# Performance work log

Measured on AMD Instinct MI355X. Metric: run time of the kernel, lower is better.

Reference implementation:

```python
import jax, jax.numpy as jnp
import numpy as np

VOCAB = 100000
D = 128
B = 256
L = 2048  # leaves per tree (power of two -> complete binary tree)


def setup_inputs() -> dict:
    key = jax.random.key(0)
    k1, k2, k3, k4 = jax.random.split(key, 4)
    word_ids = jax.random.randint(k1, (B, L), 0, VOCAB)
    embedding = jax.random.normal(k2, (VOCAB, D), dtype=jnp.float32) * 0.1
    # torch nn.Linear(2*D, D): weight [D, 2*D], bias [D]
    W = jax.random.normal(k3, (D, 2 * D), dtype=jnp.float32) * (1.0 / np.sqrt(2 * D))
    b = jax.random.normal(k4, (D,), dtype=jnp.float32) * 0.01
    return {"word_ids": word_ids, "embedding": embedding, "W": W, "b": b}


def reference(word_ids, embedding, W, b):
    # Leaves: embedding lookup for every leaf of every tree. [B, L, D]
    x = embedding[word_ids]
    # Internal nodes, batched by depth: each level combines adjacent pairs
    # via linear(concat(left, right)). log2(L) levels (static unroll).
    while x.shape[1] > 1:
        left = x[:, 0::2, :]   # [B, n/2, D]
        right = x[:, 1::2, :]  # [B, n/2, D]
        pair = jnp.concatenate([left, right], axis=-1)  # [B, n/2, 2D]
        x = jnp.einsum('bnd,od->bno', pair, W) + b      # [B, n/2, D]
    return x[:, 0, :]  # root result per tree, [B, D]
```

## Files before the change

### kernel.cpp

```cpp
#include <hip/hip_runtime.h>


typedef __bf16 bf16x8 __attribute__((ext_vector_type(8)));
typedef __bf16 bf16x4 __attribute__((ext_vector_type(4)));
typedef float f32x4 __attribute__((ext_vector_type(4)));

#define STRIDE 136

__global__ void pack_w_kernel(const float* __restrict__ W,
                              __bf16* __restrict__ wpack) {
    const int f = blockIdx.x;
    const int tid = threadIdx.x;
    const int wv = tid >> 6, l = tid & 63;
    const int nl = f >> 3, kk = f & 7;
    const int o = ((wv << 1) + nl) * 16 + (l & 15);
    const int d = kk * 32 + ((l >> 4) << 3);
    const float* src = W + o * 256 + d;
    bf16x8 h;
#pragma unroll
    for (int j = 0; j < 8; ++j) h[j] = (__bf16)src[j];
    *(bf16x8*)(wpack + (size_t)(f * 256 + tid) * 8) = h;
}

__device__ __forceinline__ void step32(
    const __bf16* src0, const __bf16* src1, __bf16* dst,
    const bf16x8* wf, const float* bval, int wv, int q, int lm)
{
    f32x4 acc[2][2];
#pragma unroll
    for (int mt = 0; mt < 2; ++mt)
#pragma unroll
        for (int nl = 0; nl < 2; ++nl)
            acc[mt][nl] = f32x4{ bval[nl], bval[nl], bval[nl], bval[nl] };
#pragma unroll
    for (int kh = 0; kh < 2; ++kh) {
        const int row = 2 * lm + kh;
        bf16x8 a0[4], a1[4];
#pragma unroll
        for (int j = 0; j < 4; ++j) {
            a0[j] = *(const bf16x8*)&src0[row * STRIDE + j * 32 + q * 8];
            a1[j] = *(const bf16x8*)&src1[row * STRIDE + j * 32 + q * 8];
        }
#pragma unroll
        for (int j = 0; j < 4; ++j) {
            acc[0][0] = __builtin_amdgcn_mfma_f32_16x16x32_bf16(
                a0[j], wf[0 * 8 + kh * 4 + j], acc[0][0], 0, 0, 0);
            acc[1][0] = __builtin_amdgcn_mfma_f32_16x16x32_bf16(
                a1[j], wf[0 * 8 + kh * 4 + j], acc[1][0], 0, 0, 0);
            acc[0][1] = __builtin_amdgcn_mfma_f32_16x16x32_bf16(
                a0[j], wf[1 * 8 + kh * 4 + j], acc[0][1], 0, 0, 0);
            acc[1][1] = __builtin_amdgcn_mfma_f32_16x16x32_bf16(
                a1[j], wf[1 * 8 + kh * 4 + j], acc[1][1], 0, 0, 0);
        }
    }
#pragma unroll
    for (int mt = 0; mt < 2; ++mt)
#pragma unroll
        for (int nl = 0; nl < 2; ++nl) {
            const int col = (2 * wv + nl) * 16 + lm;
            const bf16x4 hv = __builtin_convertvector(acc[mt][nl], bf16x4);
#pragma unroll
            for (int r = 0; r < 4; ++r)
                dst[(mt * 16 + q * 4 + r) * STRIDE + col] = hv[r];
        }
    __syncthreads();
}

template <int NOUT>
__device__ __forceinline__ void step_small(
    const __bf16* src, __bf16* dst,
    const bf16x8* wf, const float* bval, int wv, int q, int lm)
{
    const int me = (NOUT >= 16) ? lm : (lm < NOUT ? lm : 0);
    f32x4 acc[2];
    acc[0] = f32x4{ bval[0], bval[0], bval[0], bval[0] };
    acc[1] = f32x4{ bval[1], bval[1], bval[1], bval[1] };
#pragma unroll
    for (int kh = 0; kh < 2; ++kh) {
        const int row = 2 * me + kh;
        bf16x8 af[4];
#pragma unroll
        for (int j = 0; j < 4; ++j)
            af[j] = *(const bf16x8*)&src[row * STRIDE + j * 32 + q * 8];
#pragma unroll
        for (int nl = 0; nl < 2; ++nl)
#pragma unroll
            for (int j = 0; j < 4; ++j)
                acc[nl] = __builtin_amdgcn_mfma_f32_16x16x32_bf16(
                    af[j], wf[nl * 8 + kh * 4 + j], acc[nl], 0, 0, 0);
    }
#pragma unroll
    for (int nl = 0; nl < 2; ++nl) {
        const int col = (2 * wv + nl) * 16 + lm;
        const bf16x4 hv = __builtin_convertvector(acc[nl], bf16x4);
#pragma unroll
        for (int r = 0; r < 4; ++r) {
            const int row = q * 4 + r;
            if (row < NOUT)
                dst[row * STRIDE + col] = hv[r];
        }
    }
    __syncthreads();
}

__device__ __forceinline__ void final4(
    const __bf16* src, __bf16* yrow,
    const bf16x8* wf, const float* bval, int wv, int q, int lm)
{
    const int me = (lm < 4) ? lm : 0;
    f32x4 acc[2];
    acc[0] = f32x4{ bval[0], bval[0], bval[0], bval[0] };
    acc[1] = f32x4{ bval[1], bval[1], bval[1], bval[1] };
#pragma unroll
    for (int kh = 0; kh < 2; ++kh) {
        const int row = 2 * me + kh;
        bf16x8 af[4];
#pragma unroll
        for (int j = 0; j < 4; ++j)
            af[j] = *(const bf16x8*)&src[row * STRIDE + j * 32 + q * 8];
#pragma unroll
        for (int nl = 0; nl < 2; ++nl)
#pragma unroll
            for (int j = 0; j < 4; ++j)
                acc[nl] = __builtin_amdgcn_mfma_f32_16x16x32_bf16(
                    af[j], wf[nl * 8 + kh * 4 + j], acc[nl], 0, 0, 0);
    }
#pragma unroll
    for (int nl = 0; nl < 2; ++nl) {
        const int col = (2 * wv + nl) * 16 + lm;
        if (q == 0) {
#pragma unroll
            for (int r = 0; r < 4; ++r)
                yrow[r * 128 + col] = (__bf16)acc[nl][r];
        }
    }
}

__device__ __forceinline__ void gather_issue(
    const int* wb64, const float* emb, int tid, f32x4 (&s)[8])
{
#pragma unroll
    for (int i = 0; i < 8; ++i) {
        const int id = wb64[(tid >> 5) + 8 * i];
        s[i] = *(const f32x4*)(emb + (size_t)id * 128 + (tid & 31) * 4);
    }
}

__device__ __forceinline__ void gather_write(
    __bf16* dst, int tid, const f32x4 (&s)[8])
{
#pragma unroll
    for (int i = 0; i < 8; ++i) {
        const int row = (tid >> 5) + 8 * i;
        *(bf16x4*)&dst[row * STRIDE + (tid & 31) * 4] =
            __builtin_convertvector(s[i], bf16x4);
    }
}

__global__ __launch_bounds__(256, 3) void tree128_kernel(
    const int* __restrict__ wid, const float* __restrict__ emb,
    const __bf16* __restrict__ wpack, const float* __restrict__ bias,
    __bf16* __restrict__ yout)
{
    __shared__ __align__(16) __bf16 bufA[64 * STRIDE];
    __shared__ __align__(16) __bf16 bufB[64 * STRIDE];
    __shared__ __align__(16) __bf16 bufD[64 * STRIDE];
    const int tid = threadIdx.x;
    const int batch = blockIdx.x >> 3;
    const int pair = blockIdx.x & 7;
    const int wv = tid >> 6, ln = tid & 63, q = ln >> 4, lm = ln & 15;

    bf16x8 wf[16];
    const bf16x8* wp = (const bf16x8*)wpack;
#pragma unroll
    for (int f = 0; f < 16; ++f) wf[f] = wp[f * 256 + tid];
    float bval[2];
    bval[0] = bias[(2 * wv + 0) * 16 + lm];
    bval[1] = bias[(2 * wv + 1) * 16 + lm];

    const int* wb = wid + batch * 2048 + pair * 256;
    f32x4 st[8];

    gather_issue(wb, emb, tid, st);
    gather_write(bufA, tid, st);
    __syncthreads();
    gather_issue(wb + 64, emb, tid, st);
    step32(bufA, bufA + 32 * STRIDE, bufB, wf, bval, wv, q, lm);
    gather_write(bufA, tid, st);
    __syncthreads();
    gather_issue(wb + 128, emb, tid, st);
    step32(bufA, bufA + 32 * STRIDE, bufB + 32 * STRIDE, wf, bval, wv, q, lm);
    gather_write(bufA, tid, st);
    step32(bufB, bufB + 32 * STRIDE, bufD, wf, bval, wv, q, lm);
    gather_issue(wb + 192, emb, tid, st);
    step32(bufA, bufA + 32 * STRIDE, bufB, wf, bval, wv, q, lm);
    gather_write(bufA, tid, st);
    __syncthreads();
    step32(bufA, bufA + 32 * STRIDE, bufB + 32 * STRIDE, wf, bval, wv, q, lm);
    step32(bufB, bufB + 32 * STRIDE, bufD + 32 * STRIDE, wf, bval, wv, q, lm);
    step32(bufD, bufD + 32 * STRIDE, bufB, wf, bval, wv, q, lm);
    step_small<16>(bufB, bufD, wf, bval, wv, q, lm);
    step_small<8>(bufD, bufB, wf, bval, wv, q, lm);
    final4(bufB, yout + (size_t)(batch * 32 + pair * 4) * 128,
           wf, bval, wv, q, lm);
}

__global__ __launch_bounds__(256) void tree32_kernel(
    const __bf16* __restrict__ yin, const __bf16* __restrict__ wpack,
    const float* __restrict__ bias, float* __restrict__ out)
{
    __shared__ __align__(16) __bf16 buf0[32 * STRIDE];
    __shared__ __align__(16) __bf16 buf1[16 * STRIDE];
    const int tid = threadIdx.x;
    const int batch = blockIdx.x;
    const int wv = tid >> 6, ln = tid & 63, q = ln >> 4, lm = ln & 15;

    bf16x8 wf[16];
    const bf16x8* wp = (const bf16x8*)wpack;
#pragma unroll
    for (int f = 0; f < 16; ++f) wf[f] = wp[f * 256 + tid];
    float bval[2];
    bval[0] = bias[(2 * wv + 0) * 16 + lm];
    bval[1] = bias[(2 * wv + 1) * 16 + lm];

#pragma unroll
    for (int i = 0; i < 2; ++i) {
        const int flat = tid + 256 * i;
        const int row = flat >> 4;
        const int c8 = flat & 15;
        const bf16x8 v =
            *(const bf16x8*)(yin + (size_t)(batch * 32 + row) * 128 + c8 * 8);
        *(bf16x8*)&buf0[row * STRIDE + c8 * 8] = v;
    }
    __syncthreads();

    step_small<16>(buf0, buf1, wf, bval, wv, q, lm);
    step_small<8> (buf1, buf0, wf, bval, wv, q, lm);
    step_small<4> (buf0, buf1, wf, bval, wv, q, lm);
    step_small<2> (buf1, buf0, wf, bval, wv, q, lm);

    {
        f32x4 acc[2];
        acc[0] = f32x4{ bval[0], bval[0], bval[0], bval[0] };
        acc[1] = f32x4{ bval[1], bval[1], bval[1], bval[1] };
#pragma unroll
        for (int kh = 0; kh < 2; ++kh) {
            bf16x8 af[4];
#pragma unroll
            for (int j = 0; j < 4; ++j)
                af[j] = *(const bf16x8*)&buf0[kh * STRIDE + j * 32 + q * 8];
#pragma unroll
            for (int nl = 0; nl < 2; ++nl)
#pragma unroll
                for (int j = 0; j < 4; ++j)
                    acc[nl] = __builtin_amdgcn_mfma_f32_16x16x32_bf16(
                        af[j], wf[nl * 8 + kh * 4 + j], acc[nl], 0, 0, 0);
        }
#pragma unroll
        for (int nl = 0; nl < 2; ++nl) {
            const int col = (2 * wv + nl) * 16 + lm;
            if (q == 0) out[(size_t)batch * 128 + col] = acc[nl][0];
        }
    }
}

extern "C" void kernel_launch(void* const* d_in, const int* in_sizes, int n_in,
                              void* d_out, int out_size, void* d_ws, size_t ws_size,
                              hipStream_t stream) {
    const int*   wid = (const int*)d_in[0];
    const float* emb = (const float*)d_in[1];
    const float* W   = (const float*)d_in[2];
    const float* b   = (const float*)d_in[3];
    float* out = (float*)d_out;

    __bf16* wpack = (__bf16*)d_ws;
    __bf16* y     = wpack + 32768;

    pack_w_kernel<<<16, 256, 0, stream>>>(W, wpack);
    tree128_kernel<<<2048, 256, 0, stream>>>(wid, emb, wpack, b, y);
    tree32_kernel<<<256, 256, 0, stream>>>(y, wpack, b, out);
}
```

Before: 130.1 us.

## Pre-convert embedding table to bf16 and gather bf16 rows in tree kernel

```diff
diff --git a/kernel.cpp b/kernel.cpp
--- a/kernel.cpp
+++ b/kernel.cpp
@@ -7,19 +7,35 @@
 
 #define STRIDE 136
 
-__global__ void pack_w_kernel(const float* __restrict__ W,
-                              __bf16* __restrict__ wpack) {
-    const int f = blockIdx.x;
+__global__ void prep_kernel(const float* __restrict__ W,
+                            const float* __restrict__ emb,
+                            __bf16* __restrict__ wpack,
+                            __bf16* __restrict__ etab, int n8) {
     const int tid = threadIdx.x;
-    const int wv = tid >> 6, l = tid & 63;
-    const int nl = f >> 3, kk = f & 7;
-    const int o = ((wv << 1) + nl) * 16 + (l & 15);
-    const int d = kk * 32 + ((l >> 4) << 3);
-    const float* src = W + o * 256 + d;
-    bf16x8 h;
-#pragma unroll
-    for (int j = 0; j < 8; ++j) h[j] = (__bf16)src[j];
-    *(bf16x8*)(wpack + (size_t)(f * 256 + tid) * 8) = h;
+    if (blockIdx.x < 16) {
+        const int f = blockIdx.x;
+        const int wv = tid >> 6, l = tid & 63;
+        const int nl = f >> 3, kk = f & 7;
+        const int o = ((wv << 1) + nl) * 16 + (l & 15);
+        const int d = kk * 32 + ((l >> 4) << 3);
+        const float* src = W + o * 256 + d;
+        bf16x8 h;
+#pragma unroll
+        for (int j = 0; j < 8; ++j) h[j] = (__bf16)src[j];
+        *(bf16x8*)(wpack + (size_t)(f * 256 + tid) * 8) = h;
+    }
+    const int stride = gridDim.x * blockDim.x;
+    for (int i = blockIdx.x * blockDim.x + tid; i < n8; i += stride) {
+        const float* s = emb + (size_t)i * 8;
+        const f32x4 a = *(const f32x4*)s;
+        const f32x4 b = *(const f32x4*)(s + 4);
+        const bf16x4 ha = __builtin_convertvector(a, bf16x4);
+        const bf16x4 hb = __builtin_convertvector(b, bf16x4);
+        bf16x8 h;
+#pragma unroll
+        for (int j = 0; j < 4; ++j) { h[j] = ha[j]; h[4 + j] = hb[j]; }
+        *(bf16x8*)(etab + (size_t)i * 8) = h;
+    }
 }
 
 __device__ __forceinline__ void step32(
@@ -136,7 +152,7 @@
     }
 }
 
-__device__ __forceinline__ void gather_issue(
+__device__ __forceinline__ void gather_issue_f32(
     const int* wb64, const float* emb, int tid, f32x4 (&s)[8])
 {
 #pragma unroll
@@ -145,8 +161,7 @@
         s[i] = *(const f32x4*)(emb + (size_t)id * 128 + (tid & 31) * 4);
     }
 }
-
-__device__ __forceinline__ void gather_write(
+__device__ __forceinline__ void gather_write_f32(
     __bf16* dst, int tid, const f32x4 (&s)[8])
 {
 #pragma unroll
@@ -157,10 +172,30 @@
     }
 }
 
+__device__ __forceinline__ void gather_issue_bf(
+    const int* wb64, const __bf16* etab, int tid, bf16x4 (&s)[8])
+{
+#pragma unroll
+    for (int i = 0; i < 8; ++i) {
+        const int id = wb64[(tid >> 5) + 8 * i];
+        s[i] = *(const bf16x4*)(etab + (size_t)id * 128 + (tid & 31) * 4);
+    }
+}
+__device__ __forceinline__ void gather_write_bf(
+    __bf16* dst, int tid, const bf16x4 (&s)[8])
+{
+#pragma unroll
+    for (int i = 0; i < 8; ++i) {
+        const int row = (tid >> 5) + 8 * i;
+        *(bf16x4*)&dst[row * STRIDE + (tid & 31) * 4] = s[i];
+    }
+}
+
+template <bool BF>
 __global__ __launch_bounds__(256, 3) void tree128_kernel(
     const int* __restrict__ wid, const float* __restrict__ emb,
-    const __bf16* __restrict__ wpack, const float* __restrict__ bias,
-    __bf16* __restrict__ yout)
+    const __bf16* __restrict__ etab, const __bf16* __restrict__ wpack,
+    const float* __restrict__ bias, __bf16* __restrict__ yout)
 {
     __shared__ __align__(16) __bf16 bufA[64 * STRIDE];
     __shared__ __align__(16) __bf16 bufB[64 * STRIDE];
@@ -179,22 +214,32 @@
     bval[1] = bias[(2 * wv + 1) * 16 + lm];
 
     const int* wb = wid + batch * 2048 + pair * 256;
-    f32x4 st[8];
-
-    gather_issue(wb, emb, tid, st);
-    gather_write(bufA, tid, st);
-    __syncthreads();
-    gather_issue(wb + 64, emb, tid, st);
+    f32x4 st32[8];
+    bf16x4 st16[8];
+
+    auto issue = [&](const int* p) {
+        if constexpr (BF) gather_issue_bf(p, etab, tid, st16);
+        else              gather_issue_f32(p, emb, tid, st32);
+    };
+    auto write = [&](__bf16* d) {
+        if constexpr (BF) gather_write_bf(d, tid, st16);
+        else              gather_write_f32(d, tid, st32);
+    };
+
+    issue(wb);
+    write(bufA);
+    __syncthreads();
+    issue(wb + 64);
     step32(bufA, bufA + 32 * STRIDE, bufB, wf, bval, wv, q, lm);
-    gather_write(bufA, tid, st);
-    __syncthreads();
-    gather_issue(wb + 128, emb, tid, st);
+    write(bufA);
+    __syncthreads();
+    issue(wb + 128);
     step32(bufA, bufA + 32 * STRIDE, bufB + 32 * STRIDE, wf, bval, wv, q, lm);
-    gather_write(bufA, tid, st);
+    write(bufA);
     step32(bufB, bufB + 32 * STRIDE, bufD, wf, bval, wv, q, lm);
-    gather_issue(wb + 192, emb, tid, st);
+    issue(wb + 192);
     step32(bufA, bufA + 32 * STRIDE, bufB, wf, bval, wv, q, lm);
-    gather_write(bufA, tid, st);
+    write(bufA);
     __syncthreads();
     step32(bufA, bufA + 32 * STRIDE, bufB + 32 * STRIDE, wf, bval, wv, q, lm);
     step32(bufB, bufB + 32 * STRIDE, bufD + 32 * STRIDE, wf, bval, wv, q, lm);
@@ -275,8 +320,19 @@
 
     __bf16* wpack = (__bf16*)d_ws;
     __bf16* y     = wpack + 32768;
-
-    pack_w_kernel<<<16, 256, 0, stream>>>(W, wpack);
-    tree128_kernel<<<2048, 256, 0, stream>>>(wid, emb, wpack, b, y);
+    __bf16* etab  = y + 256 * 32 * 128;
+
+    const size_t need = (size_t)32768 * 2 + (size_t)256 * 32 * 128 * 2
+                      + (size_t)100000 * 128 * 2;
+    const bool bf = (ws_size >= need);
+    const int n8 = bf ? (100000 * 128 / 8) : 0;
+
+    prep_kernel<<<bf ? 2048 : 16, 256, 0, stream>>>(W, emb, wpack, etab, n8);
+    if (bf)
+        tree128_kernel<true><<<2048, 256, 0, stream>>>(
+            wid, emb, etab, wpack, b, y);
+    else
+        tree128_kernel<false><<<2048, 256, 0, stream>>>(
+            wid, emb, etab, wpack, b, y);
     tree32_kernel<<<256, 256, 0, stream>>>(y, wpack, b, out);
 }
```

Result: no change. 131.8 us (+1.3%).
